# Optimization experiments

Measured on AMD Instinct MI355X. Metric: run time of the kernel, lower is better.

The kernel has to match this reference:

```python
import jax, jax.numpy as jnp
import numpy as np

EMBED = 1024
HEADS = 16


def setup_inputs() -> dict:
    key = jax.random.key(0)
    ks = jax.random.split(key, 12)
    s = 1.0 / np.sqrt(EMBED)
    return {
        "x": jax.random.normal(ks[0], (1, EMBED, 128, 128), jnp.float32),
        "masks": jax.random.normal(ks[1], (200, 128, 128), jnp.float32),
        "Wq": jax.random.normal(ks[2], (EMBED, EMBED), jnp.float32) * s,
        "bq": jax.random.normal(ks[3], (EMBED,), jnp.float32) * 0.02,
        "Wk": jax.random.normal(ks[4], (EMBED, EMBED), jnp.float32) * s,
        "bk": jax.random.normal(ks[5], (EMBED,), jnp.float32) * 0.02,
        "Wv": jax.random.normal(ks[6], (EMBED, EMBED), jnp.float32) * s,
        "bv": jax.random.normal(ks[7], (EMBED,), jnp.float32) * 0.02,
        "Wc": jax.random.normal(ks[8], (EMBED, EMBED), jnp.float32) * s,
        "bc": jax.random.normal(ks[9], (EMBED,), jnp.float32) * 0.02,
    }


def reference(x, masks, Wq, bq, Wk, bk, Wv, bv, Wc, bc):
    # x: [1, C, H, W], masks: [Q, H, W]  (way4 branch, batch must be 1)
    N, C, H, W = x.shape
    Q = masks.shape[0]
    HW = H * W
    nh = HEADS
    hd = C // nh

    xs = x.reshape(C, HW).T                      # [HW, C] pixel tokens
    m = jax.nn.sigmoid(masks).reshape(Q, HW).T   # [HW, Q]

    # mask-weighted mean pooling (avoid materializing [HW, Q, C])
    w = jnp.sum(m, axis=0)                       # [Q]
    mean = jnp.einsum('lq,lc->qc', m, xs) / (w[:, None] + 0.001)  # [Q, C]

    seq = jnp.concatenate([mean, xs], axis=0)    # [L, C], L = Q + HW
    L = Q + HW

    q = (mean @ Wq.T + bq).reshape(Q, nh, hd) * (hd ** -0.5)
    k = (seq @ Wk.T + bk).reshape(L, nh, hd)
    v = (seq @ Wv.T + bv).reshape(L, nh, hd)

    # bool attn mask [Q, L]: True = disallowed
    qq = ~jnp.eye(Q, dtype=bool)                 # only self among pooled queries
    qp = (m.T <= 0.9)                            # pixels with sigmoid <= 0.9 masked
    attn_mask = jnp.concatenate([qq, qp], axis=1)  # [Q, L]

    scores = jnp.einsum('qhd,lhd->hql', q, k)    # [nh, Q, L]
    scores = jnp.where(attn_mask[None], -jnp.inf, scores)
    probs = jax.nn.softmax(scores, axis=-1)
    ctx = jnp.einsum('hql,lhd->qhd', probs, v).reshape(Q, C)
    out = ctx @ Wc.T + bc                        # [Q, out_dim]
    return out.reshape(Q, 1, -1)                 # match torch [Q, batch=1, out_dim]
```

## Files before the change

kernel.cpp:

```cpp
#include <hip/hip_runtime.h>
#include <math.h>

#define HW_  16384
#define Q_   200
#define C_   1024
#define L_   16584
#define NH_  16
#define HD_  64
#define CAP  512
#define KSPLIT 8
#define KCH  (HW_ / KSPLIT)
#define ASPLIT 4
#define SK   8

typedef __attribute__((ext_vector_type(8))) __bf16 bf16x8;
typedef __attribute__((ext_vector_type(8))) unsigned short u16x8;
typedef __attribute__((ext_vector_type(4))) unsigned short u16x4;
typedef __attribute__((ext_vector_type(4))) float f32x4;

__device__ inline unsigned short f2bf(float f) {
  unsigned int u = __float_as_uint(f);
  u += 0x7fff + ((u >> 16) & 1);
  return (unsigned short)(u >> 16);
}
__device__ inline float bf2f(unsigned short u) {
  return __uint_as_float((unsigned int)u << 16);
}

__global__ __launch_bounds__(256) void k_sigmoid_w(const float* __restrict__ masks,
                                                   float* __restrict__ msig,
                                                   unsigned short* __restrict__ msigbf,
                                                   float* __restrict__ w) {
  int q = blockIdx.x;
  int tid = threadIdx.x;
  unsigned short* obf = msigbf + (size_t)q * HW_;
  if (q >= Q_) {
    u16x4 z = {0, 0, 0, 0};
    for (int i = tid; i < HW_ / 4; i += 256) *(u16x4*)&obf[i * 4] = z;
    return;
  }
  const float4* mrow4 = (const float4*)(masks + (size_t)q * HW_);
  float4* orow4 = (float4*)(msig + (size_t)q * HW_);
  float s = 0.f;
  for (int i = tid; i < HW_ / 4; i += 256) {
    float4 v = mrow4[i];
    float4 sg;
    sg.x = 1.f / (1.f + expf(-v.x));
    sg.y = 1.f / (1.f + expf(-v.y));
    sg.z = 1.f / (1.f + expf(-v.z));
    sg.w = 1.f / (1.f + expf(-v.w));
    orow4[i] = sg;
    u16x4 o = {f2bf(sg.x), f2bf(sg.y), f2bf(sg.z), f2bf(sg.w)};
    *(u16x4*)&obf[i * 4] = o;
    s += sg.x + sg.y + sg.z + sg.w;
  }
  __shared__ float red[256];
  red[tid] = s;
  __syncthreads();
  for (int off = 128; off > 0; off >>= 1) {
    if (tid < off) red[tid] += red[tid + off];
    __syncthreads();
  }
  if (tid == 0) w[q] = red[0];
}

__global__ __launch_bounds__(256) void k_compact(const float* __restrict__ msig,
                                                 int* __restrict__ cnt,
                                                 int* __restrict__ idxg) {
  int q = blockIdx.x;
  int tid = threadIdx.x;
  const float* mrow = msig + (size_t)q * HW_;
  const int CHUNK = HW_ / 256;
  int base = tid * CHUNK;
  int my = 0;
  for (int j = 0; j < CHUNK; j++) my += (mrow[base + j] > 0.9f) ? 1 : 0;
  __shared__ int sc[256];
  sc[tid] = my;
  __syncthreads();
  for (int off = 1; off < 256; off <<= 1) {
    int v = sc[tid];
    int add = (tid >= off) ? sc[tid - off] : 0;
    __syncthreads();
    sc[tid] = v + add;
    __syncthreads();
  }
  int excl = sc[tid] - my;
  int total = sc[255];
  int* orow = idxg + (size_t)q * CAP;
  int off = 1 + excl;
  for (int j = 0; j < CHUNK; j++) {
    if (mrow[base + j] > 0.9f) {
      if (off < CAP) orow[off] = Q_ + base + j;
      off++;
    }
  }
  if (tid == 0) {
    orow[0] = q;
    int c = 1 + total;
    cnt[q] = c < CAP ? c : CAP;
  }
}

__global__ __launch_bounds__(256) void k_xcast(const float* __restrict__ x,
                                               unsigned short* __restrict__ xbf,
                                               unsigned short* __restrict__ seqbf) {
  __shared__ float t[32][33];
  int l0 = blockIdx.x * 32, c0 = blockIdx.y * 32;
  int tx = threadIdx.x, ty = threadIdx.y;
  #pragma unroll
  for (int i = 0; i < 32; i += 8) {
    float v = x[(size_t)(c0 + ty + i) * HW_ + l0 + tx];
    t[ty + i][tx] = v;
    xbf[(size_t)(c0 + ty + i) * HW_ + l0 + tx] = f2bf(v);
  }
  __syncthreads();
  #pragma unroll
  for (int i = 0; i < 32; i += 8)
    seqbf[(size_t)(Q_ + l0 + ty + i) * C_ + c0 + tx] = f2bf(t[tx][ty + i]);
}

__global__ __launch_bounds__(256) void k_cast4(const float* __restrict__ s0,
                                               const float* __restrict__ s1,
                                               const float* __restrict__ s2,
                                               const float* __restrict__ s3,
                                               unsigned short* __restrict__ d0,
                                               unsigned short* __restrict__ d1,
                                               unsigned short* __restrict__ d2,
                                               unsigned short* __restrict__ d3) {
  const float* src = (blockIdx.y == 0) ? s0 : (blockIdx.y == 1) ? s1
                     : (blockIdx.y == 2) ? s2 : s3;
  unsigned short* dst = (blockIdx.y == 0) ? d0 : (blockIdx.y == 1) ? d1
                        : (blockIdx.y == 2) ? d2 : d3;
  int i = (blockIdx.x * 256 + threadIdx.x) * 4;
  float4 v = *(const float4*)&src[i];
  u16x4 o = {f2bf(v.x), f2bf(v.y), f2bf(v.z), f2bf(v.w)};
  *(u16x4*)&dst[i] = o;
}

#define GBM 128
#define GBN 128
#define GBK 32

__global__ __launch_bounds__(512) void k_gemm_kv(const unsigned short* __restrict__ A,
                                                 const unsigned short* __restrict__ Bk,
                                                 const unsigned short* __restrict__ Bv,
                                                 const float* __restrict__ bk,
                                                 const float* __restrict__ bv,
                                                 unsigned short* __restrict__ Ko,
                                                 unsigned short* __restrict__ Vo,
                                                 int M, int K) {
  __shared__ __attribute__((aligned(16))) unsigned short smem[2][3 * GBM * GBK];
  int w = blockIdx.x;
  int nbm = gridDim.x >> 3;
  int t = (w >> 3) + (w & 7) * nbm;
  int bm = (t >> 3) * GBM;
  int bn = (t & 7) * GBN;
  int tid = threadIdx.x;
  int wid = tid >> 6, lane = tid & 63;
  int w2 = wid & 3;
  int wr = w2 >> 1, wc = w2 & 1;
  int fq = lane >> 4, fr = lane & 15;
  int srow = lane >> 2;
  int scol = (lane & 3) * 8;
  int boff = (wid < 4) ? GBM * GBK : 2 * GBM * GBK;

  auto stage = [&](int buf, int k0) {
    #pragma unroll
    for (int i = 0; i < 3; i++) {
      int ci = wid * 3 + i;
      const unsigned short* src;
      if (ci < 8) {
        int gA = bm + ci * 16 + srow; if (gA > M - 1) gA = M - 1;
        src = A + (size_t)gA * K + k0 + scol;
      } else if (ci < 16) {
        src = Bk + (size_t)(bn + (ci - 8) * 16 + srow) * K + k0 + scol;
      } else {
        src = Bv + (size_t)(bn + (ci - 16) * 16 + srow) * K + k0 + scol;
      }
      __builtin_amdgcn_global_load_lds(
          (const __attribute__((address_space(1))) void*)src,
          (__attribute__((address_space(3))) void*)((char*)&smem[buf][0] + ci * 1024),
          16, 0, 0);
    }
  };

  f32x4 acc[4][4] = {};
  const int NT = K / GBK;
  stage(0, 0);
  __syncthreads();
  int cur = 0;
  for (int it = 0; it < NT; it++) {
    if (it + 1 < NT) stage(cur ^ 1, (it + 1) * GBK);
    const unsigned short (*As)[GBK]  = (const unsigned short (*)[GBK])(&smem[cur][0]);
    const unsigned short (*Bts)[GBK] = (const unsigned short (*)[GBK])(&smem[cur][0] + boff);
    bf16x8 af[4], bfr[4];
    #pragma unroll
    for (int mi = 0; mi < 4; mi++)
      af[mi] = *(const bf16x8*)&As[wr * 64 + mi * 16 + fr][fq * 8];
    #pragma unroll
    for (int ni = 0; ni < 4; ni++)
      bfr[ni] = *(const bf16x8*)&Bts[wc * 64 + ni * 16 + fr][fq * 8];
    #pragma unroll
    for (int mi = 0; mi < 4; mi++)
      #pragma unroll
      for (int ni = 0; ni < 4; ni++)
        acc[mi][ni] = __builtin_amdgcn_mfma_f32_16x16x32_bf16(bfr[ni], af[mi], acc[mi][ni], 0, 0, 0);
    __syncthreads();
    cur ^= 1;
  }
  const float* bias = (wid < 4) ? bk : bv;
  unsigned short* Cout = (wid < 4) ? Ko : Vo;
  #pragma unroll
  for (int ni = 0; ni < 4; ni++) {
    int n0 = bn + wc * 64 + ni * 16 + fq * 4;
    float4 b4 = *(const float4*)&bias[n0];
    float bb[4] = {b4.x, b4.y, b4.z, b4.w};
    #pragma unroll
    for (int mi = 0; mi < 4; mi++) {
      int m = bm + wr * 64 + mi * 16 + fr;
      if (m < M) {
        u16x4 o;
        #pragma unroll
        for (int j = 0; j < 4; j++) o[j] = f2bf(acc[mi][ni][j] + bb[j]);
        *(u16x4*)&Cout[(size_t)m * C_ + n0] = o;
      }
    }
  }
}

__global__ __launch_bounds__(256) void k_gemm_meank(const unsigned short* __restrict__ A,
                                                    const unsigned short* __restrict__ B,
                                                    float* __restrict__ partial) {
  __shared__ __attribute__((aligned(16))) unsigned short As[2][GBM][GBK];
  __shared__ __attribute__((aligned(16))) unsigned short Bs[2][GBN][GBK];
  int bm = blockIdx.y * GBM, bn = blockIdx.x * GBN;
  int kc = blockIdx.z;
  int tid = threadIdx.x;
  int wid = tid >> 6, lane = tid & 63;
  int wr = wid >> 1, wc = wid & 1;
  int fq = lane >> 4, fr = lane & 15;
  int srow = lane >> 2;
  int scol = (lane & 3) * 8;

  auto stage = [&](int buf, int k0) {
    #pragma unroll
    for (int i = 0; i < 2; i++) {
      int r = wid * 32 + i * 16 + srow;
      __builtin_amdgcn_global_load_lds(
          (const __attribute__((address_space(1))) void*)(A + (size_t)(bm + r) * HW_ + k0 + scol),
          (__attribute__((address_space(3))) void*)((char*)&As[buf][0][0] + (wid * 2 + i) * 1024),
          16, 0, 0);
      __builtin_amdgcn_global_load_lds(
          (const __attribute__((address_space(1))) void*)(B + (size_t)(bn + r) * HW_ + k0 + scol),
          (__attribute__((address_space(3))) void*)((char*)&Bs[buf][0][0] + (wid * 2 + i) * 1024),
          16, 0, 0);
    }
  };

  f32x4 acc[4][4] = {};
  int kbeg = kc * KCH;
  const int NT = KCH / GBK;
  stage(0, kbeg);
  __syncthreads();
  int cur = 0;
  for (int it = 0; it < NT; it++) {
    if (it + 1 < NT) stage(cur ^ 1, kbeg + (it + 1) * GBK);
    bf16x8 af[4], bfr[4];
    #pragma unroll
    for (int mi = 0; mi < 4; mi++)
      af[mi] = *(const bf16x8*)&As[cur][wr * 64 + mi * 16 + fr][fq * 8];
    #pragma unroll
    for (int ni = 0; ni < 4; ni++)
      bfr[ni] = *(const bf16x8*)&Bs[cur][wc * 64 + ni * 16 + fr][fq * 8];
    #pragma unroll
    for (int mi = 0; mi < 4; mi++)
      #pragma unroll
      for (int ni = 0; ni < 4; ni++)
        acc[mi][ni] = __builtin_amdgcn_mfma_f32_16x16x32_bf16(bfr[ni], af[mi], acc[mi][ni], 0, 0, 0);
    __syncthreads();
    cur ^= 1;
  }
  #pragma unroll
  for (int ni = 0; ni < 4; ni++) {
    int n0 = bn + wc * 64 + ni * 16 + fq * 4;
    #pragma unroll
    for (int mi = 0; mi < 4; mi++) {
      int m = bm + wr * 64 + mi * 16 + fr;
      *(f32x4*)&partial[((size_t)kc * 256 + m) * C_ + n0] = acc[mi][ni];
    }
  }
}

__global__ __launch_bounds__(256) void k_mean_reduce(const float* __restrict__ partial,
                                                     const float* __restrict__ w,
                                                     unsigned short* __restrict__ seqbf) {
  int m = blockIdx.x;
  float rs = 1.f / (w[m] + 0.001f);
  for (int n = threadIdx.x; n < C_; n += 256) {
    float s = 0.f;
    #pragma unroll
    for (int kc = 0; kc < KSPLIT; kc++)
      s += partial[((size_t)kc * 256 + m) * C_ + n];
    seqbf[(size_t)m * C_ + n] = f2bf(s * rs);
  }
}

__global__ __launch_bounds__(256) void k_gemm_splitk_bf(const unsigned short* __restrict__ A,
                                                        const unsigned short* __restrict__ B,
                                                        float* __restrict__ partial,
                                                        int M, int K) {
  __shared__ __attribute__((aligned(16))) unsigned short As[2][GBM][GBK];
  __shared__ __attribute__((aligned(16))) unsigned short Bs[2][GBN][GBK];
  int bm = blockIdx.y * GBM, bn = blockIdx.x * GBN;
  int kc = blockIdx.z;
  int kchunk = K / SK;
  int tid = threadIdx.x;
  int wid = tid >> 6, lane = tid & 63;
  int wr = wid >> 1, wc = wid & 1;
  int fq = lane >> 4, fr = lane & 15;
  int srow = lane >> 2;
  int scol = (lane & 3) * 8;

  auto stage = [&](int buf, int k0) {
    #pragma unroll
    for (int i = 0; i < 2; i++) {
      int r = wid * 32 + i * 16 + srow;
      int gA = bm + r; if (gA > M - 1) gA = M - 1;
      __builtin_amdgcn_global_load_lds(
          (const __attribute__((address_space(1))) void*)(A + (size_t)gA * K + k0 + scol),
          (__attribute__((address_space(3))) void*)((char*)&As[buf][0][0] + (wid * 2 + i) * 1024),
          16, 0, 0);
      __builtin_amdgcn_global_load_lds(
          (const __attribute__((address_space(1))) void*)(B + (size_t)(bn + r) * K + k0 + scol),
          (__attribute__((address_space(3))) void*)((char*)&Bs[buf][0][0] + (wid * 2 + i) * 1024),
          16, 0, 0);
    }
  };

  f32x4 acc[4][4] = {};
  int kbeg = kc * kchunk;
  const int NT = kchunk / GBK;
  stage(0, kbeg);
  __syncthreads();
  int cur = 0;
  for (int it = 0; it < NT; it++) {
    if (it + 1 < NT) stage(cur ^ 1, kbeg + (it + 1) * GBK);
    bf16x8 af[4], bfr[4];
    #pragma unroll
    for (int mi = 0; mi < 4; mi++)
      af[mi] = *(const bf16x8*)&As[cur][wr * 64 + mi * 16 + fr][fq * 8];
    #pragma unroll
    for (int ni = 0; ni < 4; ni++)
      bfr[ni] = *(const bf16x8*)&Bs[cur][wc * 64 + ni * 16 + fr][fq * 8];
    #pragma unroll
    for (int mi = 0; mi < 4; mi++)
      #pragma unroll
      for (int ni = 0; ni < 4; ni++)
        acc[mi][ni] = __builtin_amdgcn_mfma_f32_16x16x32_bf16(bfr[ni], af[mi], acc[mi][ni], 0, 0, 0);
    __syncthreads();
    cur ^= 1;
  }
  #pragma unroll
  for (int ni = 0; ni < 4; ni++) {
    int n0 = bn + wc * 64 + ni * 16 + fq * 4;
    #pragma unroll
    for (int mi = 0; mi < 4; mi++) {
      int m = bm + wr * 64 + mi * 16 + fr;
      *(f32x4*)&partial[((size_t)kc * 256 + m) * C_ + n0] = acc[mi][ni];
    }
  }
}

__global__ __launch_bounds__(256) void k_splitk_reduce(const float* __restrict__ partial,
                                                       const float* __restrict__ bias,
                                                       float* __restrict__ outf) {
  int m = blockIdx.x;
  for (int n = threadIdx.x; n < C_; n += 256) {
    float s = 0.f;
    #pragma unroll
    for (int kc = 0; kc < SK; kc++)
      s += partial[((size_t)kc * 256 + m) * C_ + n];
    outf[(size_t)m * C_ + n] = s + bias[n];
  }
}

__global__ __launch_bounds__(256) void k_attn_split(const float* __restrict__ qb,
                                                    const unsigned short* __restrict__ kb,
                                                    const unsigned short* __restrict__ vb,
                                                    const int* __restrict__ cnt_g,
                                                    const int* __restrict__ idxg,
                                                    float* __restrict__ pmax,
                                                    float* __restrict__ psum,
                                                    float* __restrict__ pacc) {
  int q = blockIdx.x, h = blockIdx.y, sp = blockIdx.z;
  int tid = threadIdx.x;
  int lane = tid & 63, wid = tid >> 6;

  __shared__ float qs[64];
  __shared__ float sc[CAP / ASPLIT];
  __shared__ int   ls[CAP / ASPLIT];
  __shared__ float wred[4];
  __shared__ float accb[4][64];

  int cnt = cnt_g[q];
  int cq = (cnt + ASPLIT - 1) / ASPLIT;
  int beg = sp * cq;
  int end = beg + cq; if (end > cnt) end = cnt;
  int ns = end - beg; if (ns < 0) ns = 0;

  if (tid < 64) qs[tid] = qb[(size_t)q * C_ + h * HD_ + tid] * 0.125f;
  __syncthreads();

  if (tid < ns) {
    int l = idxg[(size_t)q * CAP + beg + tid];
    ls[tid] = l;
    const u16x8* kr = (const u16x8*)(kb + (size_t)l * C_ + h * HD_);
    float s = 0.f;
    #pragma unroll
    for (int v8 = 0; v8 < 8; v8++) {
      u16x8 kv = kr[v8];
      #pragma unroll
      for (int e = 0; e < 8; e++) s = fmaf(qs[v8 * 8 + e], bf2f(kv[e]), s);
    }
    sc[tid] = s;
  }
  __syncthreads();

  float lm = (tid < ns) ? sc[tid] : -INFINITY;
  #pragma unroll
  for (int off = 32; off; off >>= 1) lm = fmaxf(lm, __shfl_xor(lm, off));
  if (lane == 0) wred[wid] = lm;
  __syncthreads();
  float m4 = fmaxf(fmaxf(wred[0], wred[1]), fmaxf(wred[2], wred[3]));

  float e = 0.f;
  if (tid < ns) {
    e = expf(sc[tid] - m4);
    sc[tid] = e;
  }
  float lsum = e;
  #pragma unroll
  for (int off = 32; off; off >>= 1) lsum += __shfl_xor(lsum, off);
  __syncthreads();
  if (lane == 0) wred[wid] = lsum;
  __syncthreads();
  float S4 = wred[0] + wred[1] + wred[2] + wred[3];

  float acc = 0.f;
  for (int j = wid; j < ns; j += 4)
    acc = fmaf(sc[j], bf2f(vb[(size_t)ls[j] * C_ + h * HD_ + lane]), acc);
  accb[wid][lane] = acc;
  __syncthreads();

  int pidx = (q * NH_ + h) * ASPLIT + sp;
  if (tid < 64)
    pacc[(size_t)pidx * 64 + tid] =
        accb[0][tid] + accb[1][tid] + accb[2][tid] + accb[3][tid];
  if (tid == 0) {
    pmax[pidx] = (ns > 0) ? m4 : -INFINITY;
    psum[pidx] = S4;
  }
}

__global__ __launch_bounds__(64) void k_attn_merge(const float* __restrict__ pmax,
                                                   const float* __restrict__ psum,
                                                   const float* __restrict__ pacc,
                                                   unsigned short* __restrict__ ctxbf) {
  int q = blockIdx.x, h = blockIdx.y;
  int d = threadIdx.x;
  int base = (q * NH_ + h) * ASPLIT;
  float M = -INFINITY;
  #pragma unroll
  for (int s = 0; s < ASPLIT; s++) M = fmaxf(M, pmax[base + s]);
  float S = 0.f, a = 0.f;
  #pragma unroll
  for (int s = 0; s < ASPLIT; s++) {
    float wgt = expf(pmax[base + s] - M);
    S += psum[base + s] * wgt;
    a += pacc[(size_t)(base + s) * 64 + d] * wgt;
  }
  ctxbf[(size_t)q * C_ + h * HD_ + d] = f2bf(a / S);
}

extern "C" void kernel_launch(void* const* d_in, const int* in_sizes, int n_in,
                              void* d_out, int out_size, void* d_ws, size_t ws_size,
                              hipStream_t stream) {
  const float* x     = (const float*)d_in[0];
  const float* masks = (const float*)d_in[1];
  const float* Wq    = (const float*)d_in[2];
  const float* bq    = (const float*)d_in[3];
  const float* Wk    = (const float*)d_in[4];
  const float* bk    = (const float*)d_in[5];
  const float* Wv    = (const float*)d_in[6];
  const float* bv    = (const float*)d_in[7];
  const float* Wc    = (const float*)d_in[8];
  const float* bc    = (const float*)d_in[9];
  float* out = (float*)d_out;

  char* p = (char*)d_ws;
  auto alloc = [&](size_t bytes) {
    char* r = p;
    p += (bytes + 255) & ~(size_t)255;
    return r;
  };
  float* msig    = (float*)alloc((size_t)Q_ * HW_ * 4);
  float* w       = (float*)alloc(1024);
  float* qbuf    = (float*)alloc((size_t)Q_ * C_ * 4);
  float* partial = (float*)alloc((size_t)KSPLIT * 256 * C_ * 4);
  int*   cnt     = (int*)alloc(1024);
  int*   idxg    = (int*)alloc((size_t)Q_ * CAP * 4);
  float* pmax    = (float*)alloc((size_t)Q_ * NH_ * ASPLIT * 4);
  float* psum    = (float*)alloc((size_t)Q_ * NH_ * ASPLIT * 4);
  float* pacc    = (float*)alloc((size_t)Q_ * NH_ * ASPLIT * 64 * 4);
  unsigned short* msigbf = (unsigned short*)alloc((size_t)256 * HW_ * 2);
  unsigned short* xbf    = (unsigned short*)alloc((size_t)C_ * HW_ * 2);
  unsigned short* seqbf  = (unsigned short*)alloc((size_t)L_ * C_ * 2);
  unsigned short* wkbf   = (unsigned short*)alloc((size_t)C_ * C_ * 2);
  unsigned short* wvbf   = (unsigned short*)alloc((size_t)C_ * C_ * 2);
  unsigned short* wqbf   = (unsigned short*)alloc((size_t)C_ * C_ * 2);
  unsigned short* wcbf   = (unsigned short*)alloc((size_t)C_ * C_ * 2);
  unsigned short* ctxbf  = (unsigned short*)alloc((size_t)256 * C_ * 2);
  unsigned short* kbuf   = (unsigned short*)alloc((size_t)L_ * C_ * 2);
  unsigned short* vbuf   = (unsigned short*)alloc((size_t)L_ * C_ * 2);

  k_sigmoid_w<<<256, 256, 0, stream>>>(masks, msig, msigbf, w);
  k_compact<<<Q_, 256, 0, stream>>>(msig, cnt, idxg);
  k_xcast<<<dim3(HW_ / 32, C_ / 32), dim3(32, 8), 0, stream>>>(x, xbf, seqbf);
  k_cast4<<<dim3(C_ * C_ / 1024, 4), 256, 0, stream>>>(Wk, Wv, Wq, Wc,
                                                       wkbf, wvbf, wqbf, wcbf);
  k_gemm_meank<<<dim3(C_ / GBN, 2, KSPLIT), 256, 0, stream>>>(msigbf, xbf, partial);
  k_mean_reduce<<<Q_, 256, 0, stream>>>(partial, w, seqbf);
  k_gemm_splitk_bf<<<dim3(C_ / GBN, 2, SK), 256, 0, stream>>>(seqbf, wqbf, partial, Q_, C_);
  k_splitk_reduce<<<Q_, 256, 0, stream>>>(partial, bq, qbuf);
  k_gemm_kv<<<8 * ((L_ + GBM - 1) / GBM), 512, 0, stream>>>(
      seqbf, wkbf, wvbf, bk, bv, kbuf, vbuf, L_, C_);
  k_attn_split<<<dim3(Q_, NH_, ASPLIT), 256, 0, stream>>>(
      qbuf, kbuf, vbuf, cnt, idxg, pmax, psum, pacc);
  k_attn_merge<<<dim3(Q_, NH_), 64, 0, stream>>>(pmax, psum, pacc, ctxbf);
  k_gemm_splitk_bf<<<dim3(C_ / GBN, 2, SK), 256, 0, stream>>>(ctxbf, wcbf, partial, Q_, C_);
  k_splitk_reduce<<<Q_, 256, 0, stream>>>(partial, bc, out);
}
```

Measured before the change: 311.9 us.

## Triple-buffer GEMM LDS staging with explicit vmcnt waits and raise attention split

Both bf16 GEMM kernels (KV projection and mean pooling) move from double to triple buffering of LDS tiles. Two tiles are prefetched ahead, and partial s_waitcnt vmcnt counts replace full __syncthreads drains, so global-to-LDS loads overlap more MFMA work. The attention split factor ASPLIT also goes from 4 to 8 for more parallelism. The cost is more LDS per block, which may lower occupancy, and hand-counted vmcnt values that must match the number of outstanding loads per stage.

```diff
diff --git a/kernel.cpp b/kernel.cpp
--- a/kernel.cpp
+++ b/kernel.cpp
@@ -10,7 +10,7 @@
 #define CAP  512
 #define KSPLIT 8
 #define KCH  (HW_ / KSPLIT)
-#define ASPLIT 4
+#define ASPLIT 8
 #define SK   8
 
 typedef __attribute__((ext_vector_type(8))) __bf16 bf16x8;
@@ -149,7 +149,7 @@
                                                  unsigned short* __restrict__ Ko,
                                                  unsigned short* __restrict__ Vo,
                                                  int M, int K) {
-  __shared__ __attribute__((aligned(16))) unsigned short smem[2][3 * GBM * GBK];
+  __shared__ __attribute__((aligned(16))) unsigned short smem[3][3 * GBM * GBK];
   int w = blockIdx.x;
   int nbm = gridDim.x >> 3;
   int t = (w >> 3) + (w & 7) * nbm;
@@ -187,10 +187,19 @@
   f32x4 acc[4][4] = {};
   const int NT = K / GBK;
   stage(0, 0);
-  __syncthreads();
-  int cur = 0;
+  stage(1, GBK);
   for (int it = 0; it < NT; it++) {
-    if (it + 1 < NT) stage(cur ^ 1, (it + 1) * GBK);
+    int cur = it % 3;
+    if (it + 2 < NT) {
+      stage((it + 2) % 3, (it + 2) * GBK);
+      asm volatile("s_waitcnt vmcnt(6)" ::: "memory");
+    } else if (it + 1 < NT) {
+      asm volatile("s_waitcnt vmcnt(3)" ::: "memory");
+    } else {
+      asm volatile("s_waitcnt vmcnt(0)" ::: "memory");
+    }
+    __builtin_amdgcn_s_barrier();
+    asm volatile("" ::: "memory");
     const unsigned short (*As)[GBK]  = (const unsigned short (*)[GBK])(&smem[cur][0]);
     const unsigned short (*Bts)[GBK] = (const unsigned short (*)[GBK])(&smem[cur][0] + boff);
     bf16x8 af[4], bfr[4];
@@ -205,8 +214,9 @@
       #pragma unroll
       for (int ni = 0; ni < 4; ni++)
         acc[mi][ni] = __builtin_amdgcn_mfma_f32_16x16x32_bf16(bfr[ni], af[mi], acc[mi][ni], 0, 0, 0);
-    __syncthreads();
-    cur ^= 1;
+    asm volatile("" ::: "memory");
+    __builtin_amdgcn_s_barrier();
+    asm volatile("" ::: "memory");
   }
   const float* bias = (wid < 4) ? bk : bv;
   unsigned short* Cout = (wid < 4) ? Ko : Vo;
@@ -231,8 +241,8 @@
 __global__ __launch_bounds__(256) void k_gemm_meank(const unsigned short* __restrict__ A,
                                                     const unsigned short* __restrict__ B,
                                                     float* __restrict__ partial) {
-  __shared__ __attribute__((aligned(16))) unsigned short As[2][GBM][GBK];
-  __shared__ __attribute__((aligned(16))) unsigned short Bs[2][GBN][GBK];
+  __shared__ __attribute__((aligned(16))) unsigned short As[3][GBM][GBK];
+  __shared__ __attribute__((aligned(16))) unsigned short Bs[3][GBN][GBK];
   int bm = blockIdx.y * GBM, bn = blockIdx.x * GBN;
   int kc = blockIdx.z;
   int tid = threadIdx.x;
@@ -261,10 +271,19 @@
   int kbeg = kc * KCH;
   const int NT = KCH / GBK;
   stage(0, kbeg);
-  __syncthreads();
-  int cur = 0;
+  stage(1, kbeg + GBK);
   for (int it = 0; it < NT; it++) {
-    if (it + 1 < NT) stage(cur ^ 1, kbeg + (it + 1) * GBK);
+    int cur = it % 3;
+    if (it + 2 < NT) {
+      stage((it + 2) % 3, kbeg + (it + 2) * GBK);
+      asm volatile("s_waitcnt vmcnt(8)" ::: "memory");
+    } else if (it + 1 < NT) {
+      asm volatile("s_waitcnt vmcnt(4)" ::: "memory");
+    } else {
+      asm volatile("s_waitcnt vmcnt(0)" ::: "memory");
+    }
+    __builtin_amdgcn_s_barrier();
+    asm volatile("" ::: "memory");
     bf16x8 af[4], bfr[4];
     #pragma unroll
     for (int mi = 0; mi < 4; mi++)
@@ -277,8 +296,9 @@
       #pragma unroll
       for (int ni = 0; ni < 4; ni++)
         acc[mi][ni] = __builtin_amdgcn_mfma_f32_16x16x32_bf16(bfr[ni], af[mi], acc[mi][ni], 0, 0, 0);
-    __syncthreads();
-    cur ^= 1;
+    asm volatile("" ::: "memory");
+    __builtin_amdgcn_s_barrier();
+    asm volatile("" ::: "memory");
   }
   #pragma unroll
   for (int ni = 0; ni < 4; ni++) {
```

New measurement: 329.2 us. 5.6% more time.

## Triple-buffer KV GEMM with vmcnt waits and XOR-swizzle LDS tiles

Applied to the files above, without the earlier changes.

The KV projection GEMM moves from a double-buffered to a triple-buffered LDS pipeline. Loads run two stages ahead, and explicit s_waitcnt vmcnt counts with raw barriers replace __syncthreads, so direct-to-LDS loads overlap more of the MFMA work. All three bf16 GEMM kernels now apply an XOR swizzle to the 16-byte column slot on both the global_load_lds write and the fragment reads, to reduce LDS bank conflicts. The epilogue loops are reordered. The triple buffer raises LDS use per block, which may lower occupancy, and the hand-counted vmcnt values must match the three loads issued per stage.

```diff
diff --git a/kernel.cpp b/kernel.cpp
--- a/kernel.cpp
+++ b/kernel.cpp
@@ -26,6 +26,7 @@
 __device__ inline float bf2f(unsigned short u) {
   return __uint_as_float((unsigned int)u << 16);
 }
+
 
 __global__ __launch_bounds__(256) void k_sigmoid_w(const float* __restrict__ masks,
                                                    float* __restrict__ msig,
@@ -149,7 +150,7 @@
                                                  unsigned short* __restrict__ Ko,
                                                  unsigned short* __restrict__ Vo,
                                                  int M, int K) {
-  __shared__ __attribute__((aligned(16))) unsigned short smem[2][3 * GBM * GBK];
+  __shared__ __attribute__((aligned(16))) unsigned short smem[3][3 * GBM * GBK];
   int w = blockIdx.x;
   int nbm = gridDim.x >> 3;
   int t = (w >> 3) + (w & 7) * nbm;
@@ -161,7 +162,8 @@
   int wr = w2 >> 1, wc = w2 & 1;
   int fq = lane >> 4, fr = lane & 15;
   int srow = lane >> 2;
-  int scol = (lane & 3) * 8;
+  int scol = (((lane & 3) ^ ((lane >> 3) & 3)) * 8);
+  int sslot = (fq ^ ((fr >> 1) & 3)) * 8;
   int boff = (wid < 4) ? GBM * GBK : 2 * GBM * GBK;
 
   auto stage = [&](int buf, int k0) {
@@ -187,43 +189,50 @@
   f32x4 acc[4][4] = {};
   const int NT = K / GBK;
   stage(0, 0);
-  __syncthreads();
-  int cur = 0;
+  stage(1, GBK);
   for (int it = 0; it < NT; it++) {
-    if (it + 1 < NT) stage(cur ^ 1, (it + 1) * GBK);
+    int cur = it % 3;
+    if (it + 2 < NT) {
+      stage((it + 2) % 3, (it + 2) * GBK);
+      asm volatile("s_waitcnt vmcnt(6)" ::: "memory");
+    } else if (it + 1 < NT) {
+      asm volatile("s_waitcnt vmcnt(3)" ::: "memory");
+    } else {
+      asm volatile("s_waitcnt vmcnt(0)" ::: "memory");
+    }
+    __builtin_amdgcn_s_barrier();
+    asm volatile("" ::: "memory");
     const unsigned short (*As)[GBK]  = (const unsigned short (*)[GBK])(&smem[cur][0]);
     const unsigned short (*Bts)[GBK] = (const unsigned short (*)[GBK])(&smem[cur][0] + boff);
     bf16x8 af[4], bfr[4];
     #pragma unroll
     for (int mi = 0; mi < 4; mi++)
-      af[mi] = *(const bf16x8*)&As[wr * 64 + mi * 16 + fr][fq * 8];
+      af[mi] = *(const bf16x8*)&As[wr * 64 + mi * 16 + fr][sslot];
     #pragma unroll
     for (int ni = 0; ni < 4; ni++)
-      bfr[ni] = *(const bf16x8*)&Bts[wc * 64 + ni * 16 + fr][fq * 8];
+      bfr[ni] = *(const bf16x8*)&Bts[wc * 64 + ni * 16 + fr][sslot];
     #pragma unroll
     for (int mi = 0; mi < 4; mi++)
       #pragma unroll
       for (int ni = 0; ni < 4; ni++)
         acc[mi][ni] = __builtin_amdgcn_mfma_f32_16x16x32_bf16(bfr[ni], af[mi], acc[mi][ni], 0, 0, 0);
-    __syncthreads();
-    cur ^= 1;
+    asm volatile("" ::: "memory");
+    __builtin_amdgcn_s_barrier();
+    asm volatile("" ::: "memory");
   }
   const float* bias = (wid < 4) ? bk : bv;
   unsigned short* Cout = (wid < 4) ? Ko : Vo;
   #pragma unroll
-  for (int ni = 0; ni < 4; ni++) {
-    int n0 = bn + wc * 64 + ni * 16 + fq * 4;
-    float4 b4 = *(const float4*)&bias[n0];
-    float bb[4] = {b4.x, b4.y, b4.z, b4.w};
-    #pragma unroll
-    for (int mi = 0; mi < 4; mi++) {
-      int m = bm + wr * 64 + mi * 16 + fr;
-      if (m < M) {
-        u16x4 o;
-        #pragma unroll
-        for (int j = 0; j < 4; j++) o[j] = f2bf(acc[mi][ni][j] + bb[j]);
-        *(u16x4*)&Cout[(size_t)m * C_ + n0] = o;
-      }
+  for (int mi = 0; mi < 4; mi++) {
+    int m = bm + wr * 64 + mi * 16 + fr;
+    if (m >= M) continue;
+    #pragma unroll
+    for (int ni = 0; ni < 4; ni++) {
+      int n0 = bn + wc * 64 + ni * 16 + fq * 4;
+      float4 b4 = *(const float4*)&bias[n0];
+      u16x4 o = {f2bf(acc[mi][ni][0] + b4.x), f2bf(acc[mi][ni][1] + b4.y),
+                 f2bf(acc[mi][ni][2] + b4.z), f2bf(acc[mi][ni][3] + b4.w)};
+      *(u16x4*)&Cout[(size_t)m * C_ + n0] = o;
     }
   }
 }
@@ -240,7 +249,8 @@
   int wr = wid >> 1, wc = wid & 1;
   int fq = lane >> 4, fr = lane & 15;
   int srow = lane >> 2;
-  int scol = (lane & 3) * 8;
+  int scol = (((lane & 3) ^ ((lane >> 3) & 3)) * 8);
+  int sslot = (fq ^ ((fr >> 1) & 3)) * 8;
 
   auto stage = [&](int buf, int k0) {
     #pragma unroll
@@ -268,10 +278,10 @@
     bf16x8 af[4], bfr[4];
     #pragma unroll
     for (int mi = 0; mi < 4; mi++)
-      af[mi] = *(const bf16x8*)&As[cur][wr * 64 + mi * 16 + fr][fq * 8];
+      af[mi] = *(const bf16x8*)&As[cur][wr * 64 + mi * 16 + fr][sslot];
     #pragma unroll
     for (int ni = 0; ni < 4; ni++)
-      bfr[ni] = *(const bf16x8*)&Bs[cur][wc * 64 + ni * 16 + fr][fq * 8];
+      bfr[ni] = *(const bf16x8*)&Bs[cur][wc * 64 + ni * 16 + fr][sslot];
     #pragma unroll
     for (int mi = 0; mi < 4; mi++)
       #pragma unroll
@@ -281,11 +291,11 @@
     cur ^= 1;
   }
   #pragma unroll
-  for (int ni = 0; ni < 4; ni++) {
-    int n0 = bn + wc * 64 + ni * 16 + fq * 4;
-    #pragma unroll
-    for (int mi = 0; mi < 4; mi++) {
-      int m = bm + wr * 64 + mi * 16 + fr;
+  for (int mi = 0; mi < 4; mi++) {
+    int m = bm + wr * 64 + mi * 16 + fr;
+    #pragma unroll
+    for (int ni = 0; ni < 4; ni++) {
+      int n0 = bn + wc * 64 + ni * 16 + fq * 4;
       *(f32x4*)&partial[((size_t)kc * 256 + m) * C_ + n0] = acc[mi][ni];
     }
   }
@@ -319,7 +329,8 @@
   int wr = wid >> 1, wc = wid & 1;
   int fq = lane >> 4, fr = lane & 15;
   int srow = lane >> 2;
-  int scol = (lane & 3) * 8;
+  int scol = (((lane & 3) ^ ((lane >> 3) & 3)) * 8);
+  int sslot = (fq ^ ((fr >> 1) & 3)) * 8;
 
   auto stage = [&](int buf, int k0) {
     #pragma unroll
@@ -348,10 +359,10 @@
     bf16x8 af[4], bfr[4];
     #pragma unroll
     for (int mi = 0; mi < 4; mi++)
-      af[mi] = *(const bf16x8*)&As[cur][wr * 64 + mi * 16 + fr][fq * 8];
+      af[mi] = *(const bf16x8*)&As[cur][wr * 64 + mi * 16 + fr][sslot];
     #pragma unroll
     for (int ni = 0; ni < 4; ni++)
-      bfr[ni] = *(const bf16x8*)&Bs[cur][wc * 64 + ni * 16 + fr][fq * 8];
+      bfr[ni] = *(const bf16x8*)&Bs[cur][wc * 64 + ni * 16 + fr][sslot];
     #pragma unroll
     for (int mi = 0; mi < 4; mi++)
       #pragma unroll
@@ -361,11 +372,11 @@
     cur ^= 1;
   }
   #pragma unroll
-  for (int ni = 0; ni < 4; ni++) {
-    int n0 = bn + wc * 64 + ni * 16 + fq * 4;
-    #pragma unroll
-    for (int mi = 0; mi < 4; mi++) {
-      int m = bm + wr * 64 + mi * 16 + fr;
+  for (int mi = 0; mi < 4; mi++) {
+    int m = bm + wr * 64 + mi * 16 + fr;
+    #pragma unroll
+    for (int ni = 0; ni < 4; ni++) {
+      int n0 = bn + wc * 64 + ni * 16 + fq * 4;
       *(f32x4*)&partial[((size_t)kc * 256 + m) * C_ + n0] = acc[mi][ni];
     }
   }
```

New measurement: 302.4 us. 3.0% less time.
